# Kernel tuning notes

Measured on AMD Instinct MI355X. Metric: run time of the kernel, lower is better.

The kernel has to match this reference:

```python
import jax, jax.numpy as jnp
import numpy as np

DIM_MODEL = 1024
NUM_HEADS = 16
HEAD_DIM = DIM_MODEL // NUM_HEADS


def setup_inputs() -> dict:
    key = jax.random.key(0)
    ks = jax.random.split(key, 10)
    B, S1, S2, D = 2, 1, 2048, DIM_MODEL
    q = jax.random.normal(ks[0], (B, S1, S2, 1, D), dtype=jnp.float32)
    k = jax.random.normal(ks[1], (B, S1, S2, 1, D), dtype=jnp.float32)
    v = jax.random.normal(ks[2], (B, S1, S2, 1, D), dtype=jnp.float32)
    mask = jnp.zeros((1,), dtype=jnp.bool_)
    inv_scale_factor = jnp.ones((1, 1, 1, 1), dtype=jnp.float32)
    s = 1.0 / np.sqrt(D)
    Wq = jax.random.uniform(ks[3], (D, D), jnp.float32, -s, s)
    bq = jax.random.uniform(ks[4], (D,), jnp.float32, -s, s)
    Wk = jax.random.uniform(ks[5], (D, D), jnp.float32, -s, s)
    bk = jax.random.uniform(ks[6], (D,), jnp.float32, -s, s)
    Wv = jax.random.uniform(ks[7], (D, D), jnp.float32, -s, s)
    bv = jax.random.uniform(ks[8], (D,), jnp.float32, -s, s)
    return {"q": q, "k": k, "v": v, "mask": mask, "inv_scale_factor": inv_scale_factor,
            "Wq": Wq, "bq": bq, "Wk": Wk, "bk": bk, "Wv": Wv, "bv": bv}


def reference(q, k, v, mask, inv_scale_factor, Wq, bq, Wk, bk, Wv, bv):
    # q,k,v: [B, S1, S2, 1, D]; mask is unused (faithful to source forward)
    B, S1, S2, _, D = q.shape
    H, Dh = NUM_HEADS, HEAD_DIM

    def proj(x, W, b):
        # torch Linear: x @ W.T + b, then view -> heads, transpose(2,3)
        y = jnp.einsum('bgsod,ed->bgsoe', x, W) + b  # o==1 collapses in reshape
        return jnp.swapaxes(y.reshape(B, S1, S2, H, Dh), 2, 3)  # [B,S1,H,S2,Dh]

    qh = proj(q, Wq, bq) / jnp.sqrt(jnp.asarray(Dh, q.dtype))
    kh = proj(k, Wk, bk)
    vh = proj(v, Wv, bv)

    scores = jnp.einsum('bghsd,bghtd->bghst', qh, kh) / inv_scale_factor  # [B,S1,H,S2,S2]
    p = jax.nn.softmax(scores.astype(jnp.float32), axis=-1).astype(q.dtype)
    # dropout_p=0 (eval): identity
    out = jnp.einsum('bghst,bghtd->bghsd', p, vh)  # [B,S1,H,S2,Dh]
    out = out.reshape(B, S1, H, S2 * Dh)
    out = jnp.transpose(out, (0, 1, 3, 2))  # torch transpose(2,3)
    return out.reshape(B, S1, -1)
```

## Files before the change

kernel.cpp:

```cpp
#include <hip/hip_runtime.h>
#include <stdint.h>

typedef short bf16x8 __attribute__((ext_vector_type(8)));
typedef float f32x4 __attribute__((ext_vector_type(4)));

static __device__ __forceinline__ unsigned short f2bf(float f) {
  union { float f; uint32_t u; } c; c.f = f;
  uint32_t u = c.u;
  uint32_t r = (u + 0x7fffu + ((u >> 16) & 1u)) >> 16;
  return (unsigned short)r;
}

extern "C" __device__ float __ocml_exp2_f32(float);
static __device__ __forceinline__ float exp2_(float x) {
#if __has_builtin(__builtin_amdgcn_exp2f)
  return __builtin_amdgcn_exp2f(x);
#else
  return __ocml_exp2_f32(x);
#endif
}

static __device__ __forceinline__ uint32_t cvtpk_bf16(float a, float b) {
  uint32_t r;
  asm("v_cvt_pk_bf16_f32 %0, %1, %2" : "=v"(r) : "v"(a), "v"(b));
  return r;
}

__device__ __forceinline__ void gload_lds16(const void* g, void* l) {
  __builtin_amdgcn_global_load_lds((const __attribute__((address_space(1))) uint32_t*)g,
                                   (__attribute__((address_space(3))) uint32_t*)l, 16, 0, 0);
}

__global__ __launch_bounds__(256) void k_convert(
    const float* __restrict__ q, const float* __restrict__ k, const float* __restrict__ v,
    const float* __restrict__ Wq, const float* __restrict__ Wk, const float* __restrict__ Wv,
    unsigned short* __restrict__ Xb, unsigned short* __restrict__ Wb) {
  const int NX4 = 3145728;
  const int NW4 = 786432;
  int i = blockIdx.x * 256 + threadIdx.x;
  if (i >= NX4 + NW4) return;
  const float* src; unsigned short* dst; int off4;
  if (i < NX4) {
    int a = i >> 20; off4 = i & 1048575;
    src = (a == 0) ? q : (a == 1) ? k : v;
    dst = Xb + (size_t)a * 4194304;
  } else {
    int j = i - NX4;
    int a = j >> 18; off4 = j & 262143;
    src = (a == 0) ? Wq : (a == 1) ? Wk : Wv;
    dst = Wb + (size_t)a * 1048576;
  }
  float4 f = ((const float4*)src)[off4];
  uint32_t lo = (uint32_t)f2bf(f.x) | ((uint32_t)f2bf(f.y) << 16);
  uint32_t hi = (uint32_t)f2bf(f.z) | ((uint32_t)f2bf(f.w) << 16);
  ((uint2*)dst)[off4] = make_uint2(lo, hi);
}

__global__ __launch_bounds__(256) void k_proj(
    const unsigned short* __restrict__ Xb, const unsigned short* __restrict__ Wb,
    const float* __restrict__ bq, const float* __restrict__ bk, const float* __restrict__ bv,
    const float* __restrict__ inv_scale,
    unsigned short* __restrict__ Qh, unsigned short* __restrict__ Kh,
    unsigned short* __restrict__ VhT) {
  __shared__ __align__(16) unsigned short At[128 * 32];
  __shared__ __align__(16) unsigned short Bt[128 * 32];
  const int g = blockIdx.y;
  const int m0 = (blockIdx.x >> 3) * 128, n0 = (blockIdx.x & 7) * 128;
  const unsigned short* X = Xb + (size_t)g * 4194304;
  const unsigned short* W = Wb + (size_t)g * 1048576;
  const int tid = threadIdx.x;
  const int w = tid >> 6, lane = tid & 63;
  const int wr = w >> 1, wc = w & 1;
  const int lq = lane & 15, lg = lane >> 4;

  f32x4 acc[4][4];
#pragma unroll
  for (int a = 0; a < 4; a++)
#pragma unroll
    for (int b = 0; b < 4; b++) acc[a][b] = (f32x4){0.f, 0.f, 0.f, 0.f};

  for (int kt = 0; kt < 32; ++kt) {
#pragma unroll
    for (int p = 0; p < 2; ++p) {
      int i = (w * 2 + p) * 64 + lane;
      int row = i >> 2, c = i & 3;
      gload_lds16(X + (size_t)(m0 + row) * 1024 + kt * 32 + c * 8, (char*)At + i * 16);
      gload_lds16(W + (size_t)(n0 + row) * 1024 + kt * 32 + c * 8, (char*)Bt + i * 16);
    }
    __syncthreads();
    bf16x8 af[4], bfr[4];
#pragma unroll
    for (int mi = 0; mi < 4; mi++)
      af[mi] = *(const bf16x8*)((const char*)At + ((wr * 64 + mi * 16 + lq) * 64 + lg * 16));
#pragma unroll
    for (int ni = 0; ni < 4; ni++)
      bfr[ni] = *(const bf16x8*)((const char*)Bt + ((wc * 64 + ni * 16 + lq) * 64 + lg * 16));
#pragma unroll
    for (int mi = 0; mi < 4; mi++)
#pragma unroll
      for (int ni = 0; ni < 4; ni++)
        acc[mi][ni] = __builtin_amdgcn_mfma_f32_16x16x32_bf16(af[mi], bfr[ni], acc[mi][ni], 0, 0, 0);
    __syncthreads();
  }

  const float* bias = (g == 0) ? bq : (g == 1) ? bk : bv;
  const float scale = (g == 0) ? 0.125f * 1.4426950408889634f / inv_scale[0] : 1.0f;
#pragma unroll
  for (int ni = 0; ni < 4; ni++) {
    int col = n0 + wc * 64 + ni * 16 + lq;
    float bb = bias[col];
    int h = col >> 6, dh = col & 63;
#pragma unroll
    for (int mi = 0; mi < 4; mi++) {
#pragma unroll
      for (int r = 0; r < 4; r++) {
        int row = m0 + wr * 64 + mi * 16 + lg * 4 + r;
        int b = row >> 11, s2 = row & 2047;
        unsigned short bv16 = f2bf((acc[mi][ni][r] + bb) * scale);
        if (g == 0)
          Qh[(size_t)(b * 16 + h) * 131072 + (size_t)s2 * 64 + dh] = bv16;
        else if (g == 1)
          Kh[(size_t)(b * 16 + h) * 131072 + (size_t)s2 * 64 + dh] = bv16;
        else
          VhT[(size_t)((b * 16 + h) * 64 + dh) * 2048 + s2] = bv16;
      }
    }
  }
}

__global__ __launch_bounds__(256, 2) void k_attn(
    const unsigned short* __restrict__ Qh, const unsigned short* __restrict__ Kh,
    const unsigned short* __restrict__ VhT, float* __restrict__ Ot) {
  __shared__ __align__(16) unsigned short Kt[2][64 * 64];
  __shared__ __align__(16) unsigned short Vt[2][64 * 64];
  __shared__ __align__(16) unsigned short Pl[4][32][64];
  const int n = blockIdx.x;
  const int xcd = n & 7, slot = n >> 3;
  const int bh = (xcd << 2) | (slot >> 4);
  const int qt = slot & 15;
  const int tid = threadIdx.x;
  const int w = tid >> 6, lane = tid & 63;
  const int lq = lane & 15, lg = lane >> 4;
  const int qbase = qt * 128 + w * 32;

  bf16x8 qf[2][2];
#pragma unroll
  for (int r = 0; r < 2; r++) {
    const unsigned short* qp = Qh + ((size_t)bh * 2048 + qbase + r * 16 + lq) * 64 + lg * 8;
    qf[r][0] = *(const bf16x8*)(qp);
    qf[r][1] = *(const bf16x8*)(qp + 32);
  }

  f32x4 ofr[4][2];
#pragma unroll
  for (int dt = 0; dt < 4; dt++)
#pragma unroll
    for (int r = 0; r < 2; r++) ofr[dt][r] = (f32x4){0.f, 0.f, 0.f, 0.f};
  float m[2] = {-INFINITY, -INFINITY}, l[2] = {0.f, 0.f};

  const unsigned short* kgbase = Kh + (size_t)bh * 131072;
  const unsigned short* vgbase = VhT + (size_t)bh * 64 * 2048;

#pragma unroll
  for (int p = 0; p < 2; ++p) {
    int i = p * 256 + tid;
    int row = i >> 3, c = i & 7;
    int cs = c ^ (row & 7);
    gload_lds16(kgbase + (size_t)row * 64 + cs * 8, (char*)Kt[0] + i * 16);
    gload_lds16(vgbase + (size_t)row * 2048 + cs * 8, (char*)Vt[0] + i * 16);
  }
  __syncthreads();

  for (int kv = 0; kv < 32; ++kv) {
    const int k0 = kv * 64;
    const char* ktc = (const char*)Kt[kv & 1];
    const char* vtc = (const char*)Vt[kv & 1];

    if (kv < 31) {
      char* ktn = (char*)Kt[(kv & 1) ^ 1];
      char* vtn = (char*)Vt[(kv & 1) ^ 1];
#pragma unroll
      for (int p = 0; p < 2; ++p) {
        int i = p * 256 + tid;
        int row = i >> 3, c = i & 7;
        int cs = c ^ (row & 7);
        gload_lds16(kgbase + (size_t)(k0 + 64 + row) * 64 + cs * 8, ktn + i * 16);
        gload_lds16(vgbase + (size_t)row * 2048 + (k0 + 64) + cs * 8, vtn + i * 16);
      }
    }

    f32x4 sf[4][2];
#pragma unroll
    for (int t4 = 0; t4 < 4; t4++) {
      int row = t4 * 16 + lq;
      int c0 = lg ^ (row & 7), c1 = (4 + lg) ^ (row & 7);
      bf16x8 ka = *(const bf16x8*)(ktc + row * 128 + c0 * 16);
      bf16x8 kc = *(const bf16x8*)(ktc + row * 128 + c1 * 16);
#pragma unroll
      for (int r = 0; r < 2; r++) {
        f32x4 z = (f32x4){0.f, 0.f, 0.f, 0.f};
        z = __builtin_amdgcn_mfma_f32_16x16x32_bf16(ka, qf[r][0], z, 0, 0, 0);
        z = __builtin_amdgcn_mfma_f32_16x16x32_bf16(kc, qf[r][1], z, 0, 0, 0);
        sf[t4][r] = z;
      }
    }

    float pmax[2];
#pragma unroll
    for (int r = 0; r < 2; r++) {
      float a0 = fmaxf(fmaxf(sf[0][r][0], sf[0][r][1]), fmaxf(sf[0][r][2], sf[0][r][3]));
      float a1 = fmaxf(fmaxf(sf[1][r][0], sf[1][r][1]), fmaxf(sf[1][r][2], sf[1][r][3]));
      float a2 = fmaxf(fmaxf(sf[2][r][0], sf[2][r][1]), fmaxf(sf[2][r][2], sf[2][r][3]));
      float a3 = fmaxf(fmaxf(sf[3][r][0], sf[3][r][1]), fmaxf(sf[3][r][2], sf[3][r][3]));
      float a = fmaxf(fmaxf(a0, a1), fmaxf(a2, a3));
      a = fmaxf(a, __shfl_xor(a, 16));
      a = fmaxf(a, __shfl_xor(a, 32));
      pmax[r] = a;
    }
    if (__any((pmax[0] > m[0] + 8.f) || (pmax[1] > m[1] + 8.f))) {
#pragma unroll
      for (int r = 0; r < 2; r++) {
        float mn = fmaxf(m[r], pmax[r]);
        float c = exp2_(m[r] - mn);
        m[r] = mn;
        l[r] *= c;
#pragma unroll
        for (int dt = 0; dt < 4; dt++) ofr[dt][r] *= c;
      }
    }

#pragma unroll
    for (int r = 0; r < 2; r++) {
      float ps = 0.f;
#pragma unroll
      for (int t4 = 0; t4 < 4; t4++) {
        float p0 = exp2_(sf[t4][r][0] - m[r]);
        float p1 = exp2_(sf[t4][r][1] - m[r]);
        float p2 = exp2_(sf[t4][r][2] - m[r]);
        float p3 = exp2_(sf[t4][r][3] - m[r]);
        ps += (p0 + p1) + (p2 + p3);
        uint32_t w0 = cvtpk_bf16(p0, p1);
        uint32_t w1 = cvtpk_bf16(p2, p3);
        uint64_t dw = (uint64_t)w0 | ((uint64_t)w1 << 32);
        int ch = (t4 * 2 + (lg >> 1)) ^ (lq & 7);
        __builtin_memcpy((char*)&Pl[w][r * 16 + lq][0] + ch * 16 + (lg & 1) * 8, &dw, 8);
      }
      ps += __shfl_xor(ps, 16);
      ps += __shfl_xor(ps, 32);
      l[r] += ps;
    }

    bf16x8 pf[2][2];
#pragma unroll
    for (int r = 0; r < 2; r++)
#pragma unroll
      for (int c = 0; c < 2; c++) {
        int ch = (c * 4 + lg) ^ (lq & 7);
        __builtin_memcpy(&pf[r][c], (const char*)&Pl[w][r * 16 + lq][0] + ch * 16, 16);
      }
    __builtin_amdgcn_s_setprio(1);
#pragma unroll
    for (int dt = 0; dt < 4; dt++) {
      int row = dt * 16 + lq;
      int c0 = lg ^ (row & 7), c1 = (4 + lg) ^ (row & 7);
      bf16x8 va = *(const bf16x8*)(vtc + row * 128 + c0 * 16);
      bf16x8 vc = *(const bf16x8*)(vtc + row * 128 + c1 * 16);
#pragma unroll
      for (int r = 0; r < 2; r++) {
        ofr[dt][r] = __builtin_amdgcn_mfma_f32_16x16x32_bf16(va, pf[r][0], ofr[dt][r], 0, 0, 0);
        ofr[dt][r] = __builtin_amdgcn_mfma_f32_16x16x32_bf16(vc, pf[r][1], ofr[dt][r], 0, 0, 0);
      }
    }
    __builtin_amdgcn_s_setprio(0);

    __syncthreads();
  }

  float rl[2] = {1.0f / l[0], 1.0f / l[1]};
#pragma unroll
  for (int dt = 0; dt < 4; dt++)
#pragma unroll
    for (int r = 0; r < 2; r++) {
      f32x4 o = ofr[dt][r] * rl[r];
      size_t q = qbase + r * 16 + lq;
      *(f32x4*)(Ot + ((size_t)bh * 2048 + q) * 64 + dt * 16 + lg * 4) = o;
    }
}

__global__ __launch_bounds__(256) void k_tr(const float* __restrict__ Ot,
                                            float* __restrict__ out) {
  int u = blockIdx.x * 256 + threadIdx.x;
  int h4 = u & 3, dh = (u >> 2) & 63, s2 = (u >> 8) & 2047, b = u >> 19;
  size_t base = ((size_t)(b * 16 + h4 * 4) * 2048 + s2) * 64 + dh;
  float4 o;
  o.x = Ot[base];
  o.y = Ot[base + 131072];
  o.z = Ot[base + 262144];
  o.w = Ot[base + 393216];
  ((float4*)out)[u] = o;
}

extern "C" void kernel_launch(void* const* d_in, const int* in_sizes, int n_in,
                              void* d_out, int out_size, void* d_ws, size_t ws_size,
                              hipStream_t stream) {
  const float* q   = (const float*)d_in[0];
  const float* k   = (const float*)d_in[1];
  const float* v   = (const float*)d_in[2];
  const float* inv = (const float*)d_in[4];
  const float* Wq  = (const float*)d_in[5];
  const float* bq  = (const float*)d_in[6];
  const float* Wk  = (const float*)d_in[7];
  const float* bk  = (const float*)d_in[8];
  const float* Wv  = (const float*)d_in[9];
  const float* bv  = (const float*)d_in[10];

  char* ws = (char*)d_ws;
  unsigned short* Xb  = (unsigned short*)(ws);
  unsigned short* Wb  = (unsigned short*)(ws + 25165824);
  unsigned short* Qh  = (unsigned short*)(ws + 31457280);
  unsigned short* Kh  = (unsigned short*)(ws + 39845888);
  unsigned short* VhT = (unsigned short*)(ws + 48234496);
  float*          Ot  = (float*)(ws);

  k_convert<<<15360, 256, 0, stream>>>(q, k, v, Wq, Wk, Wv, Xb, Wb);
  k_proj<<<dim3(256, 3), 256, 0, stream>>>(Xb, Wb, bq, bk, bv, inv, Qh, Kh, VhT);
  k_attn<<<512, 256, 0, stream>>>(Qh, Kh, VhT, Ot);
  k_tr<<<4096, 256, 0, stream>>>(Ot, (float*)d_out);
}
```

Baseline: 129.8 us.

## Split KV range across two wave groups per block and merge partial softmax

The attention kernel now runs 512 threads per block: two groups of four waves each process half of the key/value sequence for the same 128 queries, with double-buffered K/V tiles for both halves in one shared LDS array. At the end, one half writes its partial output, max and sum to LDS and the other merges them with rescaling before writing. The P-to-V stage is also split into two 32-column chunks interleaved with the exp computation, and the P staging layout drops the XOR swizzle. This aims to double the waves per CU and hide latency, at the cost of more LDS (80KB), an extra merge step and possible bank conflicts on the P buffer.

```diff
diff --git a/kernel.cpp b/kernel.cpp
--- a/kernel.cpp
+++ b/kernel.cpp
@@ -128,12 +128,10 @@
   }
 }
 
-__global__ __launch_bounds__(256, 2) void k_attn(
+__global__ __launch_bounds__(512, 4) void k_attn(
     const unsigned short* __restrict__ Qh, const unsigned short* __restrict__ Kh,
     const unsigned short* __restrict__ VhT, float* __restrict__ Ot) {
-  __shared__ __align__(16) unsigned short Kt[2][64 * 64];
-  __shared__ __align__(16) unsigned short Vt[2][64 * 64];
-  __shared__ __align__(16) unsigned short Pl[4][32][64];
+  __shared__ __align__(16) char lds[81920];
   const int n = blockIdx.x;
   const int xcd = n & 7, slot = n >> 3;
   const int bh = (xcd << 2) | (slot >> 4);
@@ -141,7 +139,8 @@
   const int tid = threadIdx.x;
   const int w = tid >> 6, lane = tid & 63;
   const int lq = lane & 15, lg = lane >> 4;
-  const int qbase = qt * 128 + w * 32;
+  const int qslot = w & 3, half = w >> 2;
+  const int qbase = qt * 128 + qslot * 32;
 
   bf16x8 qf[2][2];
 #pragma unroll
@@ -158,35 +157,34 @@
     for (int r = 0; r < 2; r++) ofr[dt][r] = (f32x4){0.f, 0.f, 0.f, 0.f};
   float m[2] = {-INFINITY, -INFINITY}, l[2] = {0.f, 0.f};
 
-  const unsigned short* kgbase = Kh + (size_t)bh * 131072;
-  const unsigned short* vgbase = VhT + (size_t)bh * 64 * 2048;
-
-#pragma unroll
-  for (int p = 0; p < 2; ++p) {
-    int i = p * 256 + tid;
-    int row = i >> 3, c = i & 7;
-    int cs = c ^ (row & 7);
-    gload_lds16(kgbase + (size_t)row * 64 + cs * 8, (char*)Kt[0] + i * 16);
-    gload_lds16(vgbase + (size_t)row * 2048 + cs * 8, (char*)Vt[0] + i * 16);
-  }
+  const unsigned short* kg = Kh + (size_t)bh * 131072;
+  const unsigned short* vg = VhT + (size_t)bh * 131072;
+
+  const int srow = tid >> 3;
+  const int scs = (tid & 7) ^ (srow & 7);
+
+  gload_lds16(kg + (size_t)(0 * 64 + srow) * 64 + scs * 8,  lds + 0 * 8192 + tid * 16);
+  gload_lds16(kg + (size_t)(16 * 64 + srow) * 64 + scs * 8, lds + 1 * 8192 + tid * 16);
+  gload_lds16(vg + (size_t)srow * 2048 + 0 * 64 + scs * 8,  lds + 32768 + 0 * 8192 + tid * 16);
+  gload_lds16(vg + (size_t)srow * 2048 + 16 * 64 + scs * 8, lds + 32768 + 1 * 8192 + tid * 16);
   __syncthreads();
 
-  for (int kv = 0; kv < 32; ++kv) {
-    const int k0 = kv * 64;
-    const char* ktc = (const char*)Kt[kv & 1];
-    const char* vtc = (const char*)Vt[kv & 1];
-
-    if (kv < 31) {
-      char* ktn = (char*)Kt[(kv & 1) ^ 1];
-      char* vtn = (char*)Vt[(kv & 1) ^ 1];
-#pragma unroll
-      for (int p = 0; p < 2; ++p) {
-        int i = p * 256 + tid;
-        int row = i >> 3, c = i & 7;
-        int cs = c ^ (row & 7);
-        gload_lds16(kgbase + (size_t)(k0 + 64 + row) * 64 + cs * 8, ktn + i * 16);
-        gload_lds16(vgbase + (size_t)row * 2048 + (k0 + 64) + cs * 8, vtn + i * 16);
-      }
+  char* plrow = lds + 65536 + w * 2048 + lq * 64;
+
+  for (int t = 0; t < 16; ++t) {
+    const char* kb = lds + ((t & 1) * 2 + half) * 8192;
+    const char* vb = lds + 32768 + ((t & 1) * 2 + half) * 8192;
+
+    if (t < 15) {
+      int buf = (t & 1) ^ 1;
+      gload_lds16(kg + (size_t)((t + 1) * 64 + srow) * 64 + scs * 8,
+                  lds + (buf * 2 + 0) * 8192 + tid * 16);
+      gload_lds16(kg + (size_t)((t + 17) * 64 + srow) * 64 + scs * 8,
+                  lds + (buf * 2 + 1) * 8192 + tid * 16);
+      gload_lds16(vg + (size_t)srow * 2048 + (t + 1) * 64 + scs * 8,
+                  lds + 32768 + (buf * 2 + 0) * 8192 + tid * 16);
+      gload_lds16(vg + (size_t)srow * 2048 + (t + 17) * 64 + scs * 8,
+                  lds + 32768 + (buf * 2 + 1) * 8192 + tid * 16);
     }
 
     f32x4 sf[4][2];
@@ -194,8 +192,8 @@
     for (int t4 = 0; t4 < 4; t4++) {
       int row = t4 * 16 + lq;
       int c0 = lg ^ (row & 7), c1 = (4 + lg) ^ (row & 7);
-      bf16x8 ka = *(const bf16x8*)(ktc + row * 128 + c0 * 16);
-      bf16x8 kc = *(const bf16x8*)(ktc + row * 128 + c1 * 16);
+      bf16x8 ka = *(const bf16x8*)(kb + row * 128 + c0 * 16);
+      bf16x8 kc = *(const bf16x8*)(kb + row * 128 + c1 * 16);
 #pragma unroll
       for (int r = 0; r < 2; r++) {
         f32x4 z = (f32x4){0.f, 0.f, 0.f, 0.f};
@@ -229,62 +227,88 @@
       }
     }
 
+    float ps[2] = {0.f, 0.f};
+#pragma unroll
+    for (int c = 0; c < 2; ++c) {
+      bf16x8 pf[2];
+#pragma unroll
+      for (int r = 0; r < 2; ++r) {
+#pragma unroll
+        for (int tt = 0; tt < 2; ++tt) {
+          int t4x = 2 * c + tt;
+          float p0 = exp2_(sf[t4x][r][0] - m[r]);
+          float p1 = exp2_(sf[t4x][r][1] - m[r]);
+          float p2 = exp2_(sf[t4x][r][2] - m[r]);
+          float p3 = exp2_(sf[t4x][r][3] - m[r]);
+          ps[r] += (p0 + p1) + (p2 + p3);
+          uint32_t w0 = cvtpk_bf16(p0, p1);
+          uint32_t w1 = cvtpk_bf16(p2, p3);
+          uint64_t dw = (uint64_t)w0 | ((uint64_t)w1 << 32);
+          __builtin_memcpy(plrow + r * 1024 + tt * 32 + lg * 8, &dw, 8);
+        }
+        __builtin_memcpy(&pf[r], plrow + r * 1024 + lg * 16, 16);
+      }
+      __builtin_amdgcn_s_setprio(1);
+#pragma unroll
+      for (int dt = 0; dt < 4; ++dt) {
+        int row = dt * 16 + lq;
+        int cc = (c * 4 + lg) ^ (row & 7);
+        bf16x8 v = *(const bf16x8*)(vb + row * 128 + cc * 16);
+#pragma unroll
+        for (int r = 0; r < 2; r++)
+          ofr[dt][r] = __builtin_amdgcn_mfma_f32_16x16x32_bf16(v, pf[r], ofr[dt][r], 0, 0, 0);
+      }
+      __builtin_amdgcn_s_setprio(0);
+    }
 #pragma unroll
     for (int r = 0; r < 2; r++) {
-      float ps = 0.f;
-#pragma unroll
-      for (int t4 = 0; t4 < 4; t4++) {
-        float p0 = exp2_(sf[t4][r][0] - m[r]);
-        float p1 = exp2_(sf[t4][r][1] - m[r]);
-        float p2 = exp2_(sf[t4][r][2] - m[r]);
-        float p3 = exp2_(sf[t4][r][3] - m[r]);
-        ps += (p0 + p1) + (p2 + p3);
-        uint32_t w0 = cvtpk_bf16(p0, p1);
-        uint32_t w1 = cvtpk_bf16(p2, p3);
-        uint64_t dw = (uint64_t)w0 | ((uint64_t)w1 << 32);
-        int ch = (t4 * 2 + (lg >> 1)) ^ (lq & 7);
-        __builtin_memcpy((char*)&Pl[w][r * 16 + lq][0] + ch * 16 + (lg & 1) * 8, &dw, 8);
-      }
-      ps += __shfl_xor(ps, 16);
-      ps += __shfl_xor(ps, 32);
-      l[r] += ps;
-    }
-
-    bf16x8 pf[2][2];
-#pragma unroll
-    for (int r = 0; r < 2; r++)
-#pragma unroll
-      for (int c = 0; c < 2; c++) {
-        int ch = (c * 4 + lg) ^ (lq & 7);
-        __builtin_memcpy(&pf[r][c], (const char*)&Pl[w][r * 16 + lq][0] + ch * 16, 16);
-      }
-    __builtin_amdgcn_s_setprio(1);
-#pragma unroll
-    for (int dt = 0; dt < 4; dt++) {
-      int row = dt * 16 + lq;
-      int c0 = lg ^ (row & 7), c1 = (4 + lg) ^ (row & 7);
-      bf16x8 va = *(const bf16x8*)(vtc + row * 128 + c0 * 16);
-      bf16x8 vc = *(const bf16x8*)(vtc + row * 128 + c1 * 16);
+      float p = ps[r];
+      p += __shfl_xor(p, 16);
+      p += __shfl_xor(p, 32);
+      l[r] += p;
+    }
+
+    __syncthreads();
+  }
+
+  const int qq = qslot * 32;
+  if (half == 1) {
+#pragma unroll
+    for (int dt = 0; dt < 4; dt++)
 #pragma unroll
       for (int r = 0; r < 2; r++) {
-        ofr[dt][r] = __builtin_amdgcn_mfma_f32_16x16x32_bf16(va, pf[r][0], ofr[dt][r], 0, 0, 0);
-        ofr[dt][r] = __builtin_amdgcn_mfma_f32_16x16x32_bf16(vc, pf[r][1], ofr[dt][r], 0, 0, 0);
-      }
-    }
-    __builtin_amdgcn_s_setprio(0);
-
-    __syncthreads();
-  }
-
-  float rl[2] = {1.0f / l[0], 1.0f / l[1]};
-#pragma unroll
-  for (int dt = 0; dt < 4; dt++)
+        f32x4 o = ofr[dt][r];
+        __builtin_memcpy(lds + ((qq + r * 16 + lq) * 68 + dt * 16 + lg * 4) * 4, &o, 16);
+      }
+    if (lg == 0) {
+#pragma unroll
+      for (int r = 0; r < 2; r++) {
+        float2 v2 = make_float2(m[r], l[r]);
+        __builtin_memcpy(lds + 36864 + (qq + r * 16 + lq) * 8, &v2, 8);
+      }
+    }
+  }
+  __syncthreads();
+  if (half == 0) {
 #pragma unroll
     for (int r = 0; r < 2; r++) {
-      f32x4 o = ofr[dt][r] * rl[r];
-      size_t q = qbase + r * 16 + lq;
-      *(f32x4*)(Ot + ((size_t)bh * 2048 + q) * 64 + dt * 16 + lg * 4) = o;
-    }
+      float2 m1l1;
+      __builtin_memcpy(&m1l1, lds + 36864 + (qq + r * 16 + lq) * 8, 8);
+      float mm = fmaxf(m[r], m1l1.x);
+      float c0 = exp2_(m[r] - mm), c1 = exp2_(m1l1.x - mm);
+      float L = l[r] * c0 + m1l1.y * c1;
+      float rl = 1.0f / L;
+      c0 *= rl; c1 *= rl;
+#pragma unroll
+      for (int dt = 0; dt < 4; dt++) {
+        f32x4 o1;
+        __builtin_memcpy(&o1, lds + ((qq + r * 16 + lq) * 68 + dt * 16 + lg * 4) * 4, 16);
+        f32x4 o = ofr[dt][r] * c0 + o1 * c1;
+        size_t q = qbase + r * 16 + lq;
+        *(f32x4*)(Ot + ((size_t)bh * 2048 + q) * 64 + dt * 16 + lg * 4) = o;
+      }
+    }
+  }
 }
 
 __global__ __launch_bounds__(256) void k_tr(const float* __restrict__ Ot,
@@ -324,6 +348,6 @@
 
   k_convert<<<15360, 256, 0, stream>>>(q, k, v, Wq, Wk, Wv, Xb, Wb);
   k_proj<<<dim3(256, 3), 256, 0, stream>>>(Xb, Wb, bq, bk, bv, inv, Qh, Kh, VhT);
-  k_attn<<<512, 256, 0, stream>>>(Qh, Kh, VhT, Ot);
+  k_attn<<<512, 512, 0, stream>>>(Qh, Kh, VhT, Ot);
   k_tr<<<4096, 256, 0, stream>>>(Ot, (float*)d_out);
 }
```

Result: slower. 137.3 us (+5.8%).

## Triple-buffer K/V tiles in attention with prefetch distance two

Applied to the files above, without the earlier changes.

Grows the K/V shared-memory staging from two buffers to three and issues each tile's loads two iterations ahead. Each iteration waits on the vmcnt counter for the current tile and then takes a single barrier, replacing the trailing __syncthreads. The aim is to hide global-to-LDS load latency better and cut one barrier per iteration. The extra 16KB of LDS per block may limit occupancy at two blocks per CU, and correctness now depends on the hand-set vmcnt value matching the number of loads in flight.

```diff
diff --git a/kernel.cpp b/kernel.cpp
--- a/kernel.cpp
+++ b/kernel.cpp
@@ -131,8 +131,8 @@
 __global__ __launch_bounds__(256, 2) void k_attn(
     const unsigned short* __restrict__ Qh, const unsigned short* __restrict__ Kh,
     const unsigned short* __restrict__ VhT, float* __restrict__ Ot) {
-  __shared__ __align__(16) unsigned short Kt[2][64 * 64];
-  __shared__ __align__(16) unsigned short Vt[2][64 * 64];
+  __shared__ __align__(16) unsigned short Kt[3][64 * 64];
+  __shared__ __align__(16) unsigned short Vt[3][64 * 64];
   __shared__ __align__(16) unsigned short Pl[4][32][64];
   const int n = blockIdx.x;
   const int xcd = n & 7, slot = n >> 3;
@@ -159,35 +159,35 @@
   float m[2] = {-INFINITY, -INFINITY}, l[2] = {0.f, 0.f};
 
   const unsigned short* kgbase = Kh + (size_t)bh * 131072;
-  const unsigned short* vgbase = VhT + (size_t)bh * 64 * 2048;
-
-#pragma unroll
-  for (int p = 0; p < 2; ++p) {
-    int i = p * 256 + tid;
-    int row = i >> 3, c = i & 7;
-    int cs = c ^ (row & 7);
-    gload_lds16(kgbase + (size_t)row * 64 + cs * 8, (char*)Kt[0] + i * 16);
-    gload_lds16(vgbase + (size_t)row * 2048 + cs * 8, (char*)Vt[0] + i * 16);
-  }
-  __syncthreads();
+  const unsigned short* vgbase = VhT + (size_t)bh * 131072;
+
+  auto STAGE = [&](int tile, int buf) {
+#pragma unroll
+    for (int p = 0; p < 2; ++p) {
+      int i = p * 256 + tid;
+      int row = i >> 3, c = i & 7;
+      int cs = c ^ (row & 7);
+      gload_lds16(kgbase + (size_t)(tile * 64 + row) * 64 + cs * 8, (char*)Kt[buf] + i * 16);
+      gload_lds16(vgbase + (size_t)row * 2048 + tile * 64 + cs * 8, (char*)Vt[buf] + i * 16);
+    }
+  };
+
+  STAGE(0, 0);
+  STAGE(1, 1);
 
   for (int kv = 0; kv < 32; ++kv) {
-    const int k0 = kv * 64;
-    const char* ktc = (const char*)Kt[kv & 1];
-    const char* vtc = (const char*)Vt[kv & 1];
-
-    if (kv < 31) {
-      char* ktn = (char*)Kt[(kv & 1) ^ 1];
-      char* vtn = (char*)Vt[(kv & 1) ^ 1];
-#pragma unroll
-      for (int p = 0; p < 2; ++p) {
-        int i = p * 256 + tid;
-        int row = i >> 3, c = i & 7;
-        int cs = c ^ (row & 7);
-        gload_lds16(kgbase + (size_t)(k0 + 64 + row) * 64 + cs * 8, ktn + i * 16);
-        gload_lds16(vgbase + (size_t)row * 2048 + (k0 + 64) + cs * 8, vtn + i * 16);
-      }
-    }
+    if (kv == 31) {
+      asm volatile("s_waitcnt vmcnt(0)" ::: "memory");
+    } else {
+      asm volatile("s_waitcnt vmcnt(4)" ::: "memory");
+    }
+    __builtin_amdgcn_s_barrier();
+    __builtin_amdgcn_sched_barrier(0);
+
+    if (kv < 30) STAGE(kv + 2, (kv + 2) % 3);
+
+    const char* ktc = (const char*)Kt[kv % 3];
+    const char* vtc = (const char*)Vt[kv % 3];
 
     f32x4 sf[4][2];
 #pragma unroll
@@ -272,8 +272,6 @@
       }
     }
     __builtin_amdgcn_s_setprio(0);
-
-    __syncthreads();
   }
 
   float rl[2] = {1.0f / l[0], 1.0f / l[1]};
```

Result: no change. 129.2 us (-0.5%).
